# Kernel optimization log

Hardware: AMD Instinct MI355X
Metric: run time of the kernel (lower is better)

Reference implementation:

```python
import jax, jax.numpy as jnp
import numpy as np

C = 512

def conv1x1(x, w, b):
    # x: (B,C,H,W), w: (O,C), b: (O,)
    return jnp.einsum('bchw,oc->bohw', x, w) + b[None, :, None, None]

def setup_inputs() -> dict:
    key = jax.random.key(0)
    ks = jax.random.split(key, 9)
    s = 1.0 / np.sqrt(C)
    inp = {'x': jax.random.normal(ks[0], (4, C, 64, 64), dtype=jnp.float32)}
    for i, name in enumerate(['theta', 'phi', 'g', 'out']):
        inp[f'w_{name}'] = jax.random.uniform(ks[1 + 2 * i], (C, C), jnp.float32, -s, s)
        inp[f'b_{name}'] = jax.random.uniform(ks[2 + 2 * i], (C,), jnp.float32, -s, s)
    return inp

def reference(x, w_theta, b_theta, w_phi, b_phi, w_g, b_g, w_out, b_out):
    B, Cc, H, W = x.shape
    scale = int(Cc) ** (-0.5)
    # NOTE: faithful to source — g conv is applied to x first, gn is unused
    g_norm = conv1x1(x, w_g, b_g)
    theta = conv1x1(g_norm, w_theta, b_theta).reshape(B, Cc, H * W)  # (B,C,N)
    phi = conv1x1(g_norm, w_phi, b_phi).reshape(B, Cc, H * W)        # (B,C,N)
    g = conv1x1(g_norm, w_g, b_g).reshape(B, Cc, H * W)              # (B,C,N)
    scores = jnp.einsum('bcn,bcm->bnm', theta, phi) * scale          # (B,N,N)
    wi = jax.nn.softmax(scores, axis=2)
    # z[b,c,n] = sum_m g[b,c,m] * wi[b,n,m]
    z = jnp.einsum('bcm,bnm->bcn', g, wi).reshape(B, Cc, H, W)
    return x + conv1x1(z, w_out, b_out)
```

## Files before the change

kernel.cpp:

```cpp
#include <hip/hip_runtime.h>
#include <hip/hip_bf16.h>

typedef __hip_bfloat16 bf16;
typedef __attribute__((ext_vector_type(8))) short          bf16x8;
typedef __attribute__((ext_vector_type(4))) float          f32x4;
typedef __attribute__((ext_vector_type(4))) int            i32x4;
typedef __attribute__((ext_vector_type(8))) int            i32x8;

#define C_DIM 512
#define NSP   4096

__device__ __forceinline__ unsigned char f2fp8(float x) {
  return (unsigned char)(__builtin_amdgcn_cvt_pk_fp8_f32(x, x, 0, false) & 0xFF);
}

__global__ __launch_bounds__(256) void cvt_bf16(const float* __restrict__ s,
                                                bf16* __restrict__ d) {
  const int i = (blockIdx.x * 256 + threadIdx.x) * 4;
  const float4 v = *reinterpret_cast<const float4*>(s + i);
  d[i + 0] = __float2bfloat16(v.x);
  d[i + 1] = __float2bfloat16(v.y);
  d[i + 2] = __float2bfloat16(v.z);
  d[i + 3] = __float2bfloat16(v.w);
}

__global__ __launch_bounds__(256) void transpose_x(const float* __restrict__ x,
                                                   bf16* __restrict__ xt) {
  __shared__ float tile[32][33];
  const int n0 = blockIdx.x * 32, c0 = blockIdx.y * 32, b = blockIdx.z;
  const int tx = threadIdx.x & 31, ty = threadIdx.x >> 5;
  const float* src = x + ((size_t)b * C_DIM + c0) * NSP + n0;
  #pragma unroll
  for (int i = 0; i < 32; i += 8)
    tile[ty + i][tx] = src[(size_t)(ty + i) * NSP + tx];
  __syncthreads();
  bf16* dst = xt + ((size_t)b * NSP + n0) * C_DIM + c0;
  #pragma unroll
  for (int i = 0; i < 32; i += 8)
    dst[(size_t)(ty + i) * C_DIM + tx] = __float2bfloat16(tile[tx][ty + i]);
}

__global__ __launch_bounds__(256) void lreduce(const float* __restrict__ Lp,
                                               float* __restrict__ Linv) {
  const int r = blockIdx.x * 256 + threadIdx.x;
  const float4* p = reinterpret_cast<const float4*>(Lp + (size_t)r * 64);
  float s = 0.0f;
  #pragma unroll
  for (int i = 0; i < 16; ++i) { const float4 v = p[i]; s += (v.x + v.y) + (v.z + v.w); }
  Linv[r] = 1.0f / s;
}

template<int EPI>
__global__ __launch_bounds__(256)
void gemm_nt(const bf16* __restrict__ A, const bf16* __restrict__ B,
             const float* __restrict__ bias, const float* __restrict__ resid,
             void* __restrict__ Cout,
             int K, int lda, int ldb, int ldc, float sqscale,
             const float* __restrict__ bias2, const float* __restrict__ bias3,
             void* __restrict__ Cout2, void* __restrict__ Cout3)
{
  __shared__ char smem[2][16384];
  const int gx = gridDim.x, gy = gridDim.y;
  const int nwg = gx * gy * gridDim.z;
  const int qq = nwg >> 3;
  int hw = blockIdx.x + gx * (blockIdx.y + gy * blockIdx.z);
  int lg = (hw & 7) * qq + (hw >> 3);
  const int bx = lg % gx; lg /= gx;
  const int by = lg % gy;

  const int t  = threadIdx.x;
  const int m0 = by * 128;
  const int n0 = bx * 128;
  A += (size_t)m0 * lda;
  B += (size_t)n0 * ldb;

  const int lane = t & 63;
  const int wv = t >> 6;
  const int wr = wv >> 1, wc = wv & 1;

  f32x4 acc[4][4];
  #pragma unroll
  for (int i = 0; i < 4; ++i)
    #pragma unroll
    for (int j = 0; j < 4; ++j) acc[i][j] = (f32x4)0.0f;

  auto STAGE = [&](int buf, int kt) {
    const bf16* a = A + kt * 32;
    const bf16* b = B + kt * 32;
    #pragma unroll
    for (int i = 0; i < 2; ++i) {
      const int chunk = i * 256 + t;
      const int row = chunk >> 2, gp = chunk & 3;
      const int gg = gp ^ ((row >> 1) & 3);
      __builtin_amdgcn_global_load_lds(
          (const __attribute__((address_space(1))) unsigned int*)(a + (size_t)row * lda + gg * 8),
          (__attribute__((address_space(3))) unsigned int*)(&smem[buf][chunk * 16]),
          16, 0, 0);
    }
    #pragma unroll
    for (int i = 0; i < 2; ++i) {
      const int chunk = i * 256 + t;
      const int row = chunk >> 2, gp = chunk & 3;
      const int gg = gp ^ ((row >> 1) & 3);
      __builtin_amdgcn_global_load_lds(
          (const __attribute__((address_space(1))) unsigned int*)(b + (size_t)row * ldb + gg * 8),
          (__attribute__((address_space(3))) unsigned int*)(&smem[buf][8192 + chunk * 16]),
          16, 0, 0);
    }
  };

  const int nk = K >> 5;
  STAGE(0, 0);
  int cur = 0;
  const int r16 = lane & 15;
  const int gxo = ((lane >> 4) ^ ((r16 >> 1) & 3)) * 16;
  const int arow = wr * 64 + r16;
  const int brow = wc * 64 + r16;

  for (int kt = 0; kt < nk; ++kt) {
    __syncthreads();
    if (kt + 1 < nk) STAGE(cur ^ 1, kt + 1);
    bf16x8 af[4], bg[4];
    #pragma unroll
    for (int i = 0; i < 4; ++i)
      af[i] = *reinterpret_cast<const bf16x8*>(&smem[cur][(arow + i * 16) * 64 + gxo]);
    #pragma unroll
    for (int j = 0; j < 4; ++j)
      bg[j] = *reinterpret_cast<const bf16x8*>(&smem[cur][8192 + (brow + j * 16) * 64 + gxo]);
    #pragma unroll
    for (int i = 0; i < 4; ++i)
      #pragma unroll
      for (int j = 0; j < 4; ++j)
        acc[i][j] = __builtin_amdgcn_mfma_f32_16x16x32_bf16(af[i], bg[j], acc[i][j], 0, 0, 0);
    cur ^= 1;
  }

  const int mq = (lane >> 4) * 4;
  const int nc = lane & 15;
  #pragma unroll
  for (int i = 0; i < 4; ++i) {
    #pragma unroll
    for (int j = 0; j < 4; ++j) {
      const int mm = m0 + wr * 64 + i * 16 + mq;
      const int nn = n0 + wc * 64 + j * 16 + nc;
      const f32x4 v = acc[i][j];
      if (EPI == 0) {
        const float bi = bias[nn];
        bf16* o = (bf16*)Cout;
        #pragma unroll
        for (int q = 0; q < 4; ++q)
          o[(size_t)(mm + q) * ldc + nn] = __float2bfloat16(v[q] + bi);
      } else if (EPI == 4) {
        const float bi = bias[nn];
        const int b = mm >> 12, ms = mm & (NSP - 1);
        const size_t off = ((size_t)b * C_DIM + nn) * NSP + ms;
        float* o = (float*)Cout + off;
        const float* r = resid + off;
        #pragma unroll
        for (int q = 0; q < 4; ++q) o[q] = v[q] + bi + r[q];
      } else {
        const int sec = nn >> 9;
        const int nl  = nn & 511;
        if (sec == 0) {
          const float bi = bias[nl];
          unsigned char* o = (unsigned char*)Cout;
          #pragma unroll
          for (int q = 0; q < 4; ++q)
            o[(size_t)(mm + q) * 512 + nl] = f2fp8((v[q] + bi) * sqscale);
        } else if (sec == 1) {
          const float bi = bias2[nl];
          unsigned char* o = (unsigned char*)Cout2;
          #pragma unroll
          for (int q = 0; q < 4; ++q)
            o[(size_t)(mm + q) * 512 + nl] = f2fp8((v[q] + bi) * sqscale);
        } else {
          const float bi = bias3[nl];
          const int b = mm >> 12, ms = mm & (NSP - 1);
          unsigned int pk = __builtin_amdgcn_cvt_pk_fp8_f32(v[0] + bi, v[1] + bi, 0, false);
          pk = __builtin_amdgcn_cvt_pk_fp8_f32(v[2] + bi, v[3] + bi, pk, true);
          *(unsigned int*)((unsigned char*)Cout3 + ((size_t)b * C_DIM + nl) * NSP + ms) = pk;
        }
      }
    }
  }
}

template<int EPI>
__global__ __launch_bounds__(256)
void gemm_f8(const unsigned char* __restrict__ A, const unsigned char* __restrict__ B,
             void* __restrict__ Cout, int K, int lda, int ldb, int ldc,
             long sA, long sB, long sC, float* __restrict__ aux)
{
  __shared__ char smem[2][32768];
  const int gx = gridDim.x, gy = gridDim.y;
  const int nwg = gx * gy * gridDim.z;
  const int qq = nwg >> 3;
  int hw = blockIdx.x + gx * (blockIdx.y + gy * blockIdx.z);
  int lg = (hw & 7) * qq + (hw >> 3);
  const int bx = lg % gx; lg /= gx;
  const int by = lg % gy;
  const int bz = lg / gy;

  const int t  = threadIdx.x;
  const int m0 = by * 128;
  const int n0 = bx * 128;
  A += (size_t)bz * sA + (size_t)m0 * lda;
  B += (size_t)bz * sB + (size_t)n0 * ldb;

  const int lane = t & 63;
  const int wv = t >> 6;
  const int wr = wv >> 1, wc = wv & 1;
  const int r16 = lane & 15, g4 = lane >> 4;

  f32x4 acc[4][4];
  #pragma unroll
  for (int i = 0; i < 4; ++i)
    #pragma unroll
    for (int j = 0; j < 4; ++j) acc[i][j] = (f32x4)0.0f;

  auto STAGE = [&](int buf, int kt) {
    const unsigned char* a = A + kt * 128;
    const unsigned char* b = B + kt * 128;
    #pragma unroll
    for (int i = 0; i < 4; ++i) {
      const int chunk = i * 256 + t;
      const int row = chunk >> 3, gp = chunk & 7;
      const int gg = gp ^ (row & 7);
      __builtin_amdgcn_global_load_lds(
          (const __attribute__((address_space(1))) unsigned int*)(a + (size_t)row * lda + gg * 16),
          (__attribute__((address_space(3))) unsigned int*)(&smem[buf][chunk * 16]),
          16, 0, 0);
    }
    #pragma unroll
    for (int i = 0; i < 4; ++i) {
      const int chunk = i * 256 + t;
      const int row = chunk >> 3, gp = chunk & 7;
      const int gg = gp ^ (row & 7);
      __builtin_amdgcn_global_load_lds(
          (const __attribute__((address_space(1))) unsigned int*)(b + (size_t)row * ldb + gg * 16),
          (__attribute__((address_space(3))) unsigned int*)(&smem[buf][16384 + chunk * 16]),
          16, 0, 0);
    }
  };

  const int nk = K >> 7;
  STAGE(0, 0);
  int cur = 0;
  const int p0 = g4 * 2;

  for (int kt = 0; kt < nk; ++kt) {
    __syncthreads();
    if (kt + 1 < nk) STAGE(cur ^ 1, kt + 1);
    i32x8 af[4], bg[4];
    #pragma unroll
    for (int i = 0; i < 4; ++i) {
      const int row = wr * 64 + i * 16 + r16;
      const i32x4 lo = *(const i32x4*)(&smem[cur][row * 128 + ((p0    ) ^ (row & 7)) * 16]);
      const i32x4 hi = *(const i32x4*)(&smem[cur][row * 128 + ((p0 + 1) ^ (row & 7)) * 16]);
      #pragma unroll
      for (int q = 0; q < 4; ++q) { af[i][q] = lo[q]; af[i][4 + q] = hi[q]; }
    }
    #pragma unroll
    for (int j = 0; j < 4; ++j) {
      const int row = wc * 64 + j * 16 + r16;
      const i32x4 lo = *(const i32x4*)(&smem[cur][16384 + row * 128 + ((p0    ) ^ (row & 7)) * 16]);
      const i32x4 hi = *(const i32x4*)(&smem[cur][16384 + row * 128 + ((p0 + 1) ^ (row & 7)) * 16]);
      #pragma unroll
      for (int q = 0; q < 4; ++q) { bg[j][q] = lo[q]; bg[j][4 + q] = hi[q]; }
    }
    #pragma unroll
    for (int i = 0; i < 4; ++i)
      #pragma unroll
      for (int j = 0; j < 4; ++j)
        acc[i][j] = __builtin_amdgcn_mfma_scale_f32_16x16x128_f8f6f4(
            af[i], bg[j], acc[i][j], 0, 0, 0, 0x7F7F7F7Fu, 0, 0x7F7F7F7Fu);
    cur ^= 1;
  }

  const int mq = g4 * 4;
  #pragma unroll
  for (int i = 0; i < 4; ++i) {
    float rs[4] = {0.0f, 0.0f, 0.0f, 0.0f};
    #pragma unroll
    for (int j = 0; j < 4; ++j) {
      const int mm = m0 + wr * 64 + i * 16 + mq;
      const int nn = n0 + wc * 64 + j * 16 + r16;
      const f32x4 v = acc[i][j];
      if (EPI == 0) {
        unsigned char* o = (unsigned char*)Cout + (size_t)bz * sC;
        #pragma unroll
        for (int q = 0; q < 4; ++q) {
          const float e = __expf(v[q]);
          o[(size_t)(mm + q) * ldc + nn] = f2fp8(e);
          rs[q] += e;
        }
      } else {
        bf16* o = (bf16*)Cout;
        #pragma unroll
        for (int q = 0; q < 4; ++q) {
          const float li = aux[(size_t)bz * NSP + mm + q];
          o[((size_t)bz * NSP + mm + q) * 512 + nn] = __float2bfloat16(v[q] * li);
        }
      }
    }
    if (EPI == 0) {
      #pragma unroll
      for (int msk = 1; msk < 16; msk <<= 1)
        #pragma unroll
        for (int q = 0; q < 4; ++q) rs[q] += __shfl_xor(rs[q], msk);
      if (r16 == 0) {
        const int mm = m0 + wr * 64 + i * 16 + mq;
        #pragma unroll
        for (int q = 0; q < 4; ++q)
          aux[((size_t)bz * NSP + mm + q) * 64 + bx * 2 + wc] = rs[q];
      }
    }
  }
}

extern "C" void kernel_launch(void* const* d_in, const int* in_sizes, int n_in,
                              void* d_out, int out_size, void* d_ws, size_t ws_size,
                              hipStream_t stream)
{
  const float* x     = (const float*)d_in[0];
  const float* w_th  = (const float*)d_in[1];
  const float* b_th  = (const float*)d_in[2];
  const float* w_ph  = (const float*)d_in[3];
  const float* b_ph  = (const float*)d_in[4];
  const float* w_g   = (const float*)d_in[5];
  const float* b_g   = (const float*)d_in[6];
  const float* w_out = (const float*)d_in[7];
  const float* b_out = (const float*)d_in[8];

  const size_t NC = (size_t)16384 * C_DIM;
  char* p = (char*)d_ws;
  auto take = [&](size_t bytes) {
    char* r = p; p += (bytes + 255) & ~(size_t)255; return r;
  };
  bf16* XT  = (bf16*)take(NC * 2);
  bf16* YT  = (bf16*)take(NC * 2);
  bf16* ZT  = (bf16*)take(NC * 2);
  unsigned char* TH8 = (unsigned char*)take(NC);
  unsigned char* PH8 = (unsigned char*)take(NC);
  unsigned char* G8  = (unsigned char*)take(NC);
  unsigned char* P8  = (unsigned char*)take((size_t)4 * NSP * NSP);
  bf16* WCAT = (bf16*)take((size_t)1536 * 512 * 2);
  bf16* WG   = (bf16*)take((size_t)512 * 512 * 2);
  bf16* WOUT = (bf16*)take((size_t)512 * 512 * 2);
  float* Lp  = (float*)take((size_t)4 * NSP * 64 * 4);
  float* Li  = (float*)take((size_t)4 * NSP * 4);

  const dim3 blk(256);
  const float sqscale = 0.21022410381342864f;
  const long sact = (long)NSP * C_DIM;
  const long sS   = (long)NSP * NSP;

  cvt_bf16<<<dim3(256), blk, 0, stream>>>(w_th,  WCAT);
  cvt_bf16<<<dim3(256), blk, 0, stream>>>(w_ph,  WCAT + (size_t)512 * 512);
  cvt_bf16<<<dim3(256), blk, 0, stream>>>(w_g,   WCAT + (size_t)1024 * 512);
  cvt_bf16<<<dim3(256), blk, 0, stream>>>(w_g,   WG);
  cvt_bf16<<<dim3(256), blk, 0, stream>>>(w_out, WOUT);

  transpose_x<<<dim3(NSP / 32, C_DIM / 32, 4), blk, 0, stream>>>(x, XT);

  gemm_nt<0><<<dim3(4, 128), blk, 0, stream>>>(XT, WG, b_g, nullptr, YT,
      512, 512, 512, 512, 1.0f, nullptr, nullptr, nullptr, nullptr);
  gemm_nt<5><<<dim3(12, 128), blk, 0, stream>>>(YT, WCAT, b_th, nullptr, TH8,
      512, 512, 512, 512, sqscale, b_ph, b_g, PH8, G8);

  gemm_f8<0><<<dim3(32, 32, 4), blk, 0, stream>>>(TH8, PH8, P8,
      512, 512, 512, NSP, sact, sact, sS, Lp);
  lreduce<<<dim3(64), blk, 0, stream>>>(Lp, Li);
  gemm_f8<1><<<dim3(4, 32, 4), blk, 0, stream>>>(P8, G8, ZT,
      4096, 4096, 4096, 512, sS, sact, 0, Li);

  gemm_nt<4><<<dim3(4, 128), blk, 0, stream>>>(ZT, WOUT, b_out, x, d_out,
      512, 512, 512, 512, 1.0f, nullptr, nullptr, nullptr, nullptr);
}
```

Before: 277.7 us.

## Precompose g-conv into theta/phi/g weights and deepen GEMM prefetch pipelining

Folds the first g 1x1 conv into the theta/phi/g weights by computing W·Wg and the composed biases, so the large activation GEMM producing YT is removed and theta/phi/g come straight from x. Both GEMM kernels now prefetch two stages ahead with explicit vmcnt waits and split barriers, replacing one __syncthreads per iteration. The bf16 composed weights add rounding error, and the manual waitcnt counts must match the number of loads issued per stage.

```diff
diff --git a/kernel.cpp b/kernel.cpp
--- a/kernel.cpp
+++ b/kernel.cpp
@@ -22,6 +22,41 @@
   d[i + 1] = __float2bfloat16(v.y);
   d[i + 2] = __float2bfloat16(v.z);
   d[i + 3] = __float2bfloat16(v.w);
+}
+
+__global__ __launch_bounds__(256) void cvt_bf16_T(const float* __restrict__ s,
+                                                  bf16* __restrict__ d) {
+  __shared__ float tile[32][33];
+  const int c0 = blockIdx.x * 32, r0 = blockIdx.y * 32;
+  const int tx = threadIdx.x & 31, ty = threadIdx.x >> 5;
+  #pragma unroll
+  for (int i = 0; i < 32; i += 8)
+    tile[ty + i][tx] = s[(size_t)(r0 + ty + i) * 512 + c0 + tx];
+  __syncthreads();
+  #pragma unroll
+  for (int i = 0; i < 32; i += 8)
+    d[(size_t)(c0 + ty + i) * 512 + r0 + tx] = __float2bfloat16(tile[tx][ty + i]);
+}
+
+__global__ __launch_bounds__(256)
+void bias_compose(const float* __restrict__ w_th, const float* __restrict__ b_th,
+                  const float* __restrict__ w_ph, const float* __restrict__ b_ph,
+                  const float* __restrict__ w_g,  const float* __restrict__ b_g,
+                  float* __restrict__ out)
+{
+  const int idx = blockIdx.x * 256 + threadIdx.x;
+  const int w = idx >> 9, o = idx & 511;
+  const float* W  = (w == 0) ? w_th : (w == 1) ? w_ph : w_g;
+  const float* bb = (w == 0) ? b_th : (w == 1) ? b_ph : b_g;
+  const float4* row = reinterpret_cast<const float4*>(W + (size_t)o * 512);
+  const float4* bg4 = reinterpret_cast<const float4*>(b_g);
+  float s = bb[o];
+  #pragma unroll 4
+  for (int i = 0; i < 128; ++i) {
+    const float4 a = row[i], c = bg4[i];
+    s += a.x * c.x + a.y * c.y + a.z * c.z + a.w * c.w;
+  }
+  out[idx] = s;
 }
 
 __global__ __launch_bounds__(256) void transpose_x(const float* __restrict__ x,
@@ -111,6 +146,7 @@
 
   const int nk = K >> 5;
   STAGE(0, 0);
+  STAGE(1, 1);
   int cur = 0;
   const int r16 = lane & 15;
   const int gxo = ((lane >> 4) ^ ((r16 >> 1) & 3)) * 16;
@@ -118,8 +154,11 @@
   const int brow = wc * 64 + r16;
 
   for (int kt = 0; kt < nk; ++kt) {
-    __syncthreads();
-    if (kt + 1 < nk) STAGE(cur ^ 1, kt + 1);
+    if (kt + 1 < nk) asm volatile("s_waitcnt vmcnt(4)" ::: "memory");
+    else             asm volatile("s_waitcnt vmcnt(0)" ::: "memory");
+    __builtin_amdgcn_sched_barrier(0);
+    __builtin_amdgcn_s_barrier();
+    __builtin_amdgcn_sched_barrier(0);
     bf16x8 af[4], bg[4];
     #pragma unroll
     for (int i = 0; i < 4; ++i)
@@ -132,6 +171,10 @@
       #pragma unroll
       for (int j = 0; j < 4; ++j)
         acc[i][j] = __builtin_amdgcn_mfma_f32_16x16x32_bf16(af[i], bg[j], acc[i][j], 0, 0, 0);
+    __builtin_amdgcn_sched_barrier(0);
+    __builtin_amdgcn_s_barrier();
+    __builtin_amdgcn_sched_barrier(0);
+    if (kt + 2 < nk) STAGE(cur, kt + 2);
     cur ^= 1;
   }
 
@@ -145,11 +188,10 @@
       const int nn = n0 + wc * 64 + j * 16 + nc;
       const f32x4 v = acc[i][j];
       if (EPI == 0) {
-        const float bi = bias[nn];
         bf16* o = (bf16*)Cout;
         #pragma unroll
         for (int q = 0; q < 4; ++q)
-          o[(size_t)(mm + q) * ldc + nn] = __float2bfloat16(v[q] + bi);
+          o[(size_t)(mm + q) * ldc + nn] = __float2bfloat16(v[q]);
       } else if (EPI == 4) {
         const float bi = bias[nn];
         const int b = mm >> 12, ms = mm & (NSP - 1);
@@ -245,12 +287,16 @@
 
   const int nk = K >> 7;
   STAGE(0, 0);
+  STAGE(1, 1);
   int cur = 0;
   const int p0 = g4 * 2;
 
   for (int kt = 0; kt < nk; ++kt) {
-    __syncthreads();
-    if (kt + 1 < nk) STAGE(cur ^ 1, kt + 1);
+    if (kt + 1 < nk) asm volatile("s_waitcnt vmcnt(8)" ::: "memory");
+    else             asm volatile("s_waitcnt vmcnt(0)" ::: "memory");
+    __builtin_amdgcn_sched_barrier(0);
+    __builtin_amdgcn_s_barrier();
+    __builtin_amdgcn_sched_barrier(0);
     i32x8 af[4], bg[4];
     #pragma unroll
     for (int i = 0; i < 4; ++i) {
@@ -274,6 +320,10 @@
       for (int j = 0; j < 4; ++j)
         acc[i][j] = __builtin_amdgcn_mfma_scale_f32_16x16x128_f8f6f4(
             af[i], bg[j], acc[i][j], 0, 0, 0, 0x7F7F7F7Fu, 0, 0x7F7F7F7Fu);
+    __builtin_amdgcn_sched_barrier(0);
+    __builtin_amdgcn_s_barrier();
+    __builtin_amdgcn_sched_barrier(0);
+    if (kt + 2 < nk) STAGE(cur, kt + 2);
     cur ^= 1;
   }
 
@@ -338,17 +388,18 @@
     char* r = p; p += (bytes + 255) & ~(size_t)255; return r;
   };
   bf16* XT  = (bf16*)take(NC * 2);
-  bf16* YT  = (bf16*)take(NC * 2);
   bf16* ZT  = (bf16*)take(NC * 2);
   unsigned char* TH8 = (unsigned char*)take(NC);
   unsigned char* PH8 = (unsigned char*)take(NC);
   unsigned char* G8  = (unsigned char*)take(NC);
   unsigned char* P8  = (unsigned char*)take((size_t)4 * NSP * NSP);
-  bf16* WCAT = (bf16*)take((size_t)1536 * 512 * 2);
-  bf16* WG   = (bf16*)take((size_t)512 * 512 * 2);
-  bf16* WOUT = (bf16*)take((size_t)512 * 512 * 2);
-  float* Lp  = (float*)take((size_t)4 * NSP * 64 * 4);
-  float* Li  = (float*)take((size_t)4 * NSP * 4);
+  bf16* WCAT  = (bf16*)take((size_t)1536 * 512 * 2);
+  bf16* WGT   = (bf16*)take((size_t)512 * 512 * 2);
+  bf16* WCATC = (bf16*)take((size_t)1536 * 512 * 2);
+  bf16* WOUT  = (bf16*)take((size_t)512 * 512 * 2);
+  float* Bc   = (float*)take((size_t)1536 * 4);
+  float* Lp   = (float*)take((size_t)4 * NSP * 64 * 4);
+  float* Li   = (float*)take((size_t)4 * NSP * 4);
 
   const dim3 blk(256);
   const float sqscale = 0.21022410381342864f;
@@ -358,15 +409,17 @@
   cvt_bf16<<<dim3(256), blk, 0, stream>>>(w_th,  WCAT);
   cvt_bf16<<<dim3(256), blk, 0, stream>>>(w_ph,  WCAT + (size_t)512 * 512);
   cvt_bf16<<<dim3(256), blk, 0, stream>>>(w_g,   WCAT + (size_t)1024 * 512);
-  cvt_bf16<<<dim3(256), blk, 0, stream>>>(w_g,   WG);
   cvt_bf16<<<dim3(256), blk, 0, stream>>>(w_out, WOUT);
+  cvt_bf16_T<<<dim3(16, 16), blk, 0, stream>>>(w_g, WGT);
+  bias_compose<<<dim3(6), blk, 0, stream>>>(w_th, b_th, w_ph, b_ph, w_g, b_g, Bc);
+
+  gemm_nt<0><<<dim3(4, 12), blk, 0, stream>>>(WCAT, WGT, nullptr, nullptr, WCATC,
+      512, 512, 512, 512, 1.0f, nullptr, nullptr, nullptr, nullptr);
 
   transpose_x<<<dim3(NSP / 32, C_DIM / 32, 4), blk, 0, stream>>>(x, XT);
 
-  gemm_nt<0><<<dim3(4, 128), blk, 0, stream>>>(XT, WG, b_g, nullptr, YT,
-      512, 512, 512, 512, 1.0f, nullptr, nullptr, nullptr, nullptr);
-  gemm_nt<5><<<dim3(12, 128), blk, 0, stream>>>(YT, WCAT, b_th, nullptr, TH8,
-      512, 512, 512, 512, sqscale, b_ph, b_g, PH8, G8);
+  gemm_nt<5><<<dim3(12, 128), blk, 0, stream>>>(XT, WCATC, Bc, nullptr, TH8,
+      512, 512, 512, 512, sqscale, Bc + 512, Bc + 1024, PH8, G8);
 
   gemm_f8<0><<<dim3(32, 32, 4), blk, 0, stream>>>(TH8, PH8, P8,
       512, 512, 512, NSP, sact, sact, sS, Lp);
```

Measured after the change: 293.4 us. 5.7% more time.
